# Kernel tuning notes

Measured on AMD Instinct MI355X. Metric: run time of the kernel, lower is better.

Reference implementation:

```python
import jax, jax.numpy as jnp
import numpy as np

N_NODES = 50000


def _gcn_conv(h, src, dst, W, b):
    # h: [N, d_in] -> [N, d_out]; symmetric-normalized aggregation with self-loops
    N = h.shape[0]
    h = h @ W  # transform first (d_out < d_in), like PyG GCNConv
    deg = jax.ops.segment_sum(jnp.ones_like(dst, dtype=h.dtype), dst, num_segments=N)
    dinv = jnp.where(deg > 0, jax.lax.rsqrt(jnp.maximum(deg, 1.0)), 0.0)
    norm = dinv[src] * dinv[dst]  # [E']
    msg = h[src] * norm[:, None]  # [E', d_out]
    out = jax.ops.segment_sum(msg, dst, num_segments=N)
    return out + b


def setup_inputs() -> dict:
    key = jax.random.key(0)
    k1, k2, k3, k4 = jax.random.split(key, 4)
    dim_in, dim_h, dim_out, E = 512, 96, 40, 800000
    x = jax.random.normal(k1, (N_NODES, dim_in), dtype=jnp.float32)
    edge_index = jax.random.randint(k2, (2, E), 0, N_NODES, dtype=jnp.int64)
    W1 = jax.random.normal(k3, (dim_in, dim_h), dtype=jnp.float32) / np.sqrt(dim_in)
    b1 = jnp.zeros((dim_h,), dtype=jnp.float32)
    W2 = jax.random.normal(k4, (dim_h, dim_out), dtype=jnp.float32) / np.sqrt(dim_h)
    b2 = jnp.zeros((dim_out,), dtype=jnp.float32)
    return {"x": x, "edge_index": edge_index, "W1": W1, "b1": b1, "W2": W2, "b2": b2}


def reference(x, edge_index, W1, b1, W2, b2):
    N = x.shape[0]
    loops = jnp.arange(N, dtype=edge_index.dtype)
    src = jnp.concatenate([edge_index[0], loops])
    dst = jnp.concatenate([edge_index[1], loops])
    h = jax.nn.relu(_gcn_conv(x, src, dst, W1, b1))
    # dropout p=0.5 is identity in eval mode (training=False)
    logits = _gcn_conv(h, src, dst, W2, b2)
    return (logits, jax.nn.log_softmax(logits, axis=1))
```

## Files before the change

### kernel.cpp

```cpp
#include <hip/hip_runtime.h>
#include <cstdint>
#include <cstddef>

#define DIN 512
#define DH  96
#define DOUT 40

typedef __attribute__((ext_vector_type(8))) short s8v;
typedef __attribute__((ext_vector_type(4))) float f4v;

__device__ __forceinline__ ushort f2bf(float f) {
    uint u = __float_as_uint(f);
    u += 0x7fffu + ((u >> 16) & 1u);
    return (ushort)(u >> 16);
}
__device__ __forceinline__ float bflo(uint u) { return __uint_as_float(u << 16); }
__device__ __forceinline__ float bfhi(uint u) { return __uint_as_float(u & 0xffff0000u); }

__global__ __launch_bounds__(256) void k_prep(
    const float* __restrict__ W1, const float* __restrict__ W2,
    int* __restrict__ cnt, ushort* __restrict__ W1T, ushort* __restrict__ W2T, int N)
{
    int i = blockIdx.x * 256 + threadIdx.x;
    if (i < N) cnt[i] = 0;
    if (i < DIN * DH) {
        int k = i / DH, n = i % DH;
        W1T[(size_t)n * DIN + k] = f2bf(W1[i]);
    }
    if (i < 48 * DH) {
        int n = i / DH, k = i % DH;
        W2T[i] = (n < DOUT) ? f2bf(W2[(size_t)k * DOUT + n]) : (ushort)0;
    }
}

__global__ __launch_bounds__(256) void k_hist(const int* __restrict__ dst, int* __restrict__ cnt, int E) {
    int e = blockIdx.x * 256 + threadIdx.x;
    if (e < E) atomicAdd(&cnt[dst[e]], 1);
}

__global__ __launch_bounds__(256) void k_blocksum(const int* __restrict__ cnt, int* __restrict__ bsum, int N) {
    int i = blockIdx.x * 256 + threadIdx.x;
    int c = (i < N) ? cnt[i] : 0;
    #pragma unroll
    for (int off = 32; off >= 1; off >>= 1) c += __shfl_down(c, off, 64);
    __shared__ int wsum[4];
    if ((threadIdx.x & 63) == 0) wsum[threadIdx.x >> 6] = c;
    __syncthreads();
    if (threadIdx.x == 0) bsum[blockIdx.x] = wsum[0] + wsum[1] + wsum[2] + wsum[3];
}

__global__ __launch_bounds__(256) void k_scan_small(const int* __restrict__ bsum, int* __restrict__ boff, int SB) {
    __shared__ int p[256];
    int tid = threadIdx.x;
    int v = (tid < SB) ? bsum[tid] : 0;
    p[tid] = v;
    __syncthreads();
    #pragma unroll
    for (int off = 1; off < 256; off <<= 1) {
        int t = (tid >= off) ? p[tid - off] : 0;
        __syncthreads();
        p[tid] += t;
        __syncthreads();
    }
    if (tid < SB) boff[tid] = p[tid] - v;
}

__global__ __launch_bounds__(256) void k_rowptr(
    const int* __restrict__ cnt, const int* __restrict__ boff,
    int* __restrict__ row_ptr, int* __restrict__ cursor,
    float* __restrict__ dinv, int N)
{
    __shared__ int p[256];
    int tid = threadIdx.x;
    int i = blockIdx.x * 256 + tid;
    int c = (i < N) ? cnt[i] : 0;
    p[tid] = c;
    __syncthreads();
    #pragma unroll
    for (int off = 1; off < 256; off <<= 1) {
        int t = (tid >= off) ? p[tid - off] : 0;
        __syncthreads();
        p[tid] += t;
        __syncthreads();
    }
    int excl = p[tid] - c;
    if (i < N) {
        int base = boff[blockIdx.x] + excl;
        row_ptr[i] = base;
        cursor[i]  = base;
        dinv[i] = rsqrtf(1.0f + (float)c);
        if (i == N - 1) row_ptr[N] = base + c;
    }
}

__global__ __launch_bounds__(256) void k_fill(
    const int* __restrict__ src, const int* __restrict__ dst,
    int* __restrict__ cursor, int* __restrict__ adj, int E)
{
    int e = blockIdx.x * 256 + threadIdx.x;
    if (e >= E) return;
    int pos = atomicAdd(&cursor[dst[e]], 1);
    adj[pos] = src[e];
}

#define G1_ASZ 8192
#define G1_BSZ 6144
__global__ __launch_bounds__(256) void k_gemm1(
    const float* __restrict__ x, const ushort* __restrict__ W1T,
    const float* __restrict__ dinv, ushort* __restrict__ hs1, int N)
{
    __shared__ ushort lds[2 * G1_ASZ + 2 * G1_BSZ];
    const int tid = threadIdx.x;
    const int row0 = blockIdx.x * 128;
    const int lane = tid & 63;
    const int w = tid >> 6;
    const int rb = (w >> 1) * 64;
    const int cb = (w & 1) * 48;
    const int lm = lane & 15;
    const int lq = lane >> 4;

    int aof[4][2], bof[3][2];
    #pragma unroll
    for (int i = 0; i < 4; ++i)
        #pragma unroll
        for (int ks = 0; ks < 2; ++ks) {
            int r = rb + i * 16 + lm;
            int c = ks * 32 + lq * 8;
            aof[i][ks] = r * 64 + (c ^ ((r & 7) << 3));
        }
    #pragma unroll
    for (int j = 0; j < 3; ++j)
        #pragma unroll
        for (int ks = 0; ks < 2; ++ks) {
            int n = cb + j * 16 + lm;
            int c = ks * 32 + lq * 8;
            bof[j][ks] = 2 * G1_ASZ + n * 64 + (c ^ ((n & 7) << 3));
        }

    f4v acc[4][3];
    #pragma unroll
    for (int i = 0; i < 4; ++i)
        #pragma unroll
        for (int j = 0; j < 3; ++j) acc[i][j] = (f4v)0.f;

    const int sr = tid >> 1;
    const int scb = (tid & 1) * 32;

    auto stage = [&](int kt, int buf) {
        int k0 = kt * 64;
        int gr = row0 + sr;
        ushort* A = lds + buf * G1_ASZ;
        #pragma unroll
        for (int s = 0; s < 4; ++s) {
            int c = scb + s * 8;
            float4 v0 = make_float4(0.f, 0.f, 0.f, 0.f), v1 = v0;
            if (gr < N) {
                const float* p = &x[(size_t)gr * DIN + k0 + c];
                v0 = *(const float4*)p;
                v1 = *(const float4*)(p + 4);
            }
            uint4 wv;
            wv.x = (uint)f2bf(v0.x) | ((uint)f2bf(v0.y) << 16);
            wv.y = (uint)f2bf(v0.z) | ((uint)f2bf(v0.w) << 16);
            wv.z = (uint)f2bf(v1.x) | ((uint)f2bf(v1.y) << 16);
            wv.w = (uint)f2bf(v1.z) | ((uint)f2bf(v1.w) << 16);
            *(uint4*)&A[sr * 64 + (c ^ ((sr & 7) << 3))] = wv;
        }
        ushort* B = lds + 2 * G1_ASZ + buf * G1_BSZ;
        #pragma unroll
        for (int it = 0; it < 3; ++it) {
            int ss = tid + it * 256;
            int n = ss >> 3, c = (ss & 7) * 8;
            uint4 wv = *(const uint4*)&W1T[(size_t)n * DIN + k0 + c];
            *(uint4*)&B[n * 64 + (c ^ ((n & 7) << 3))] = wv;
        }
    };

    stage(0, 0);
    for (int kt = 0; kt < 8; ++kt) {
        __syncthreads();
        if (kt < 7) stage(kt + 1, (kt + 1) & 1);
        const int ab = (kt & 1) * G1_ASZ;
        const int bb = (kt & 1) * G1_BSZ;
        #pragma unroll
        for (int ks = 0; ks < 2; ++ks) {
            s8v b0 = *(s8v*)&lds[bof[0][ks] + bb];
            s8v b1 = *(s8v*)&lds[bof[1][ks] + bb];
            s8v b2 = *(s8v*)&lds[bof[2][ks] + bb];
            #pragma unroll
            for (int i = 0; i < 4; ++i) {
                s8v a = *(s8v*)&lds[aof[i][ks] + ab];
                acc[i][0] = __builtin_amdgcn_mfma_f32_16x16x32_bf16(a, b0, acc[i][0], 0, 0, 0);
                acc[i][1] = __builtin_amdgcn_mfma_f32_16x16x32_bf16(a, b1, acc[i][1], 0, 0, 0);
                acc[i][2] = __builtin_amdgcn_mfma_f32_16x16x32_bf16(a, b2, acc[i][2], 0, 0, 0);
            }
        }
    }

    #pragma unroll
    for (int i = 0; i < 4; ++i) {
        int gr0 = row0 + rb + i * 16 + lq * 4;
        #pragma unroll
        for (int q = 0; q < 4; ++q) {
            int gr = gr0 + q;
            if (gr < N) {
                float di = dinv[gr];
                #pragma unroll
                for (int j = 0; j < 3; ++j)
                    hs1[(size_t)gr * DH + cb + j * 16 + lm] = f2bf(acc[i][j][q] * di);
            }
        }
    }
}

__global__ __launch_bounds__(256) void k_agg1(
    const int* __restrict__ row_ptr, const int* __restrict__ adj,
    const float* __restrict__ dinv, const ushort* __restrict__ hs1,
    const float* __restrict__ b1, ushort* __restrict__ h1, int N)
{
    int t = blockIdx.x * 256 + threadIdx.x;
    int node = t >> 6, lane = t & 63;
    if (node >= N) return;
    int c = lane << 1;
    const bool act = (c < DH);

    float a0 = 0.f, a1 = 0.f;
    if (act) {
        uint u = *(const uint*)&hs1[(size_t)node * DH + c];
        a0 = bflo(u); a1 = bfhi(u);
    }
    int e = row_ptr[node], e1 = row_ptr[node + 1];
    for (; e + 3 < e1; e += 4) {
        int s0 = adj[e], s1 = adj[e + 1], s2 = adj[e + 2], s3 = adj[e + 3];
        if (act) {
            uint u0 = *(const uint*)&hs1[(size_t)s0 * DH + c];
            uint u1 = *(const uint*)&hs1[(size_t)s1 * DH + c];
            uint u2 = *(const uint*)&hs1[(size_t)s2 * DH + c];
            uint u3 = *(const uint*)&hs1[(size_t)s3 * DH + c];
            a0 += bflo(u0); a1 += bfhi(u0);
            a0 += bflo(u1); a1 += bfhi(u1);
            a0 += bflo(u2); a1 += bfhi(u2);
            a0 += bflo(u3); a1 += bfhi(u3);
        }
    }
    for (; e < e1; ++e) {
        int s = adj[e];
        if (act) {
            uint u = *(const uint*)&hs1[(size_t)s * DH + c];
            a0 += bflo(u); a1 += bfhi(u);
        }
    }
    if (act) {
        float di = dinv[node];
        float r0 = fmaxf(fmaf(a0, di, b1[c]), 0.f);
        float r1 = fmaxf(fmaf(a1, di, b1[c + 1]), 0.f);
        uint wv = (uint)f2bf(r0) | ((uint)f2bf(r1) << 16);
        *(uint*)&h1[(size_t)node * DH + c] = wv;
    }
}

#define G2_HS 16384
__global__ __launch_bounds__(256) void k_gemm2(
    const ushort* __restrict__ h1, const ushort* __restrict__ W2T,
    const float* __restrict__ dinv, float* __restrict__ hs2, int N)
{
    __shared__ ushort lds[G2_HS + 48 * 128];
    const int tid = threadIdx.x;
    const int row0 = blockIdx.x * 128;

    for (int f = tid; f < 576; f += 256) {
        int r = f / 12, c = (f % 12) * 8;
        uint4 v = *(const uint4*)&W2T[r * DH + c];
        *(uint4*)&lds[G2_HS + r * 128 + (c ^ ((r & 7) << 3))] = v;
    }
    {
        int r = tid >> 1, half = tid & 1;
        int gr = row0 + r;
        #pragma unroll
        for (int i = 0; i < 6; ++i) {
            int c = half * 48 + i * 8;
            uint4 v = make_uint4(0, 0, 0, 0);
            if (gr < N) v = *(const uint4*)&h1[(size_t)gr * DH + c];
            *(uint4*)&lds[r * 128 + (c ^ ((r & 7) << 3))] = v;
        }
    }
    __syncthreads();

    const int lane = tid & 63, w = tid >> 6;
    const int rb = w * 32, lm = lane & 15, lq = lane >> 4;
    f4v acc[2][3];
    #pragma unroll
    for (int i = 0; i < 2; ++i)
        #pragma unroll
        for (int j = 0; j < 3; ++j) acc[i][j] = (f4v)0.f;

    #pragma unroll
    for (int ks = 0; ks < 3; ++ks) {
        int kk = ks * 32 + lq * 8;
        s8v b[3];
        #pragma unroll
        for (int j = 0; j < 3; ++j) {
            int n = j * 16 + lm;
            b[j] = *(s8v*)&lds[G2_HS + n * 128 + (kk ^ ((n & 7) << 3))];
        }
        #pragma unroll
        for (int i = 0; i < 2; ++i) {
            int r = rb + i * 16 + lm;
            s8v a = *(s8v*)&lds[r * 128 + (kk ^ ((r & 7) << 3))];
            #pragma unroll
            for (int j = 0; j < 3; ++j)
                acc[i][j] = __builtin_amdgcn_mfma_f32_16x16x32_bf16(a, b[j], acc[i][j], 0, 0, 0);
        }
    }

    #pragma unroll
    for (int i = 0; i < 2; ++i) {
        int gr0 = row0 + rb + i * 16 + lq * 4;
        #pragma unroll
        for (int q = 0; q < 4; ++q) {
            int gr = gr0 + q;
            if (gr < N) {
                float di = dinv[gr];
                #pragma unroll
                for (int j = 0; j < 3; ++j) {
                    int col = j * 16 + lm;
                    if (col < DOUT)
                        hs2[(size_t)gr * DOUT + col] = acc[i][j][q] * di;
                }
            }
        }
    }
}

__global__ __launch_bounds__(256) void k_agg2sm(
    const int* __restrict__ row_ptr, const int* __restrict__ adj,
    const float* __restrict__ dinv, const float* __restrict__ hs2,
    const float* __restrict__ b2, float* __restrict__ out,
    float* __restrict__ lsm, int N)
{
    int t = blockIdx.x * 256 + threadIdx.x;
    int node = t >> 6, lane = t & 63;
    if (node >= N) return;
    const bool act = lane < DOUT;

    float acc = act ? hs2[(size_t)node * DOUT + lane] : 0.f;
    int e = row_ptr[node], e1 = row_ptr[node + 1];
    for (; e + 3 < e1; e += 4) {
        int s0 = adj[e], s1 = adj[e + 1], s2 = adj[e + 2], s3 = adj[e + 3];
        if (act) {
            float v0 = hs2[(size_t)s0 * DOUT + lane];
            float v1 = hs2[(size_t)s1 * DOUT + lane];
            float v2 = hs2[(size_t)s2 * DOUT + lane];
            float v3 = hs2[(size_t)s3 * DOUT + lane];
            acc += v0 + v1 + v2 + v3;
        }
    }
    for (; e < e1; ++e) {
        int s = adj[e];
        if (act) acc += hs2[(size_t)s * DOUT + lane];
    }

    float v = act ? fmaf(acc, dinv[node], b2[lane]) : -1e30f;
    float m = v;
    #pragma unroll
    for (int off = 32; off >= 1; off >>= 1) m = fmaxf(m, __shfl_xor(m, off));
    float ex = act ? __expf(v - m) : 0.f;
    float s = ex;
    #pragma unroll
    for (int off = 32; off >= 1; off >>= 1) s += __shfl_xor(s, off);
    float lse = m + __logf(s);
    if (act) {
        out[(size_t)node * DOUT + lane] = v;
        lsm[(size_t)node * DOUT + lane] = v - lse;
    }
}

extern "C" void kernel_launch(void* const* d_in, const int* in_sizes, int n_in,
                              void* d_out, int out_size, void* d_ws, size_t ws_size,
                              hipStream_t stream) {
    const float* x  = (const float*)d_in[0];
    const int*   ei = (const int*)d_in[1];
    const float* W1 = (const float*)d_in[2];
    const float* b1 = (const float*)d_in[3];
    const float* W2 = (const float*)d_in[4];
    const float* b2 = (const float*)d_in[5];

    const int N = in_sizes[0] / DIN;
    const int E = in_sizes[1] / 2;
    const int* srcp = ei;
    const int* dstp = ei + E;
    const int SB = (N + 255) / 256;

    ushort* hs1 = (ushort*)d_ws;
    ushort* h1  = hs1 + (size_t)N * DH;
    float* hs2  = (float*)(h1 + (size_t)N * DH);
    float* dinv = hs2 + (size_t)N * DOUT;
    ushort* W1T = (ushort*)(dinv + N);
    ushort* W2T = W1T + (size_t)DH * DIN;
    int* cnt     = (int*)(W2T + 48 * DH);
    int* cursor  = cnt + N;
    int* row_ptr = cursor + N;
    int* adj     = row_ptr + N + 1;
    int* bsum    = adj + E;
    int* boff    = bsum + SB;

    float* out = (float*)d_out;
    float* lsm = out + (size_t)N * DOUT;

    const int gE = (E + 255) / 256;

    k_prep<<<SB, 256, 0, stream>>>(W1, W2, cnt, W1T, W2T, N);
    k_hist<<<gE, 256, 0, stream>>>(dstp, cnt, E);
    k_blocksum<<<SB, 256, 0, stream>>>(cnt, bsum, N);
    k_scan_small<<<1, 256, 0, stream>>>(bsum, boff, SB);
    k_rowptr<<<SB, 256, 0, stream>>>(cnt, boff, row_ptr, cursor, dinv, N);
    k_fill<<<gE, 256, 0, stream>>>(srcp, dstp, cursor, adj, E);

    k_gemm1<<<(N + 127) / 128, 256, 0, stream>>>(x, W1T, dinv, hs1, N);
    k_agg1<<<(int)(((size_t)N * 64 + 255) / 256), 256, 0, stream>>>(row_ptr, adj, dinv, hs1, b1, h1, N);

    k_gemm2<<<(N + 127) / 128, 256, 0, stream>>>(h1, W2T, dinv, hs2, N);
    k_agg2sm<<<(int)(((size_t)N * 64 + 255) / 256), 256, 0, stream>>>(row_ptr, adj, dinv, hs2, b2, out, lsm, N);
}
```

Measured before the change: 225.3 us.

## Record histogram slot per edge, unroll gathers by eight, use packed bf16 convert

The histogram kernel now stores each edge's atomic return value as its local slot. The fill kernel then writes adjacency entries without a second atomic pass over cursors, at the cost of an extra E-sized int array. The aggregation gather loops are unrolled from four to eight neighbours to keep more loads in flight. Float-to-bf16 packing switches to the HIP intrinsic for paired conversion.

Result: faster. 185.2 us (-17.8%).

```diff
diff --git a/kernel.cpp b/kernel.cpp
--- a/kernel.cpp
+++ b/kernel.cpp
@@ -1,4 +1,5 @@
 #include <hip/hip_runtime.h>
+#include <hip/hip_bf16.h>
 #include <cstdint>
 #include <cstddef>
 
@@ -13,6 +14,10 @@
     uint u = __float_as_uint(f);
     u += 0x7fffu + ((u >> 16) & 1u);
     return (ushort)(u >> 16);
+}
+__device__ __forceinline__ uint f2bf2(float lo, float hi) {
+    __hip_bfloat162 h = __float22bfloat162_rn(make_float2(lo, hi));
+    return *(uint*)&h;
 }
 __device__ __forceinline__ float bflo(uint u) { return __uint_as_float(u << 16); }
 __device__ __forceinline__ float bfhi(uint u) { return __uint_as_float(u & 0xffff0000u); }
@@ -33,9 +38,11 @@
     }
 }
 
-__global__ __launch_bounds__(256) void k_hist(const int* __restrict__ dst, int* __restrict__ cnt, int E) {
+__global__ __launch_bounds__(256) void k_hist(
+    const int* __restrict__ dst, int* __restrict__ cnt, int* __restrict__ pos, int E)
+{
     int e = blockIdx.x * 256 + threadIdx.x;
-    if (e < E) atomicAdd(&cnt[dst[e]], 1);
+    if (e < E) pos[e] = atomicAdd(&cnt[dst[e]], 1);
 }
 
 __global__ __launch_bounds__(256) void k_blocksum(const int* __restrict__ cnt, int* __restrict__ bsum, int N) {
@@ -67,8 +74,7 @@
 
 __global__ __launch_bounds__(256) void k_rowptr(
     const int* __restrict__ cnt, const int* __restrict__ boff,
-    int* __restrict__ row_ptr, int* __restrict__ cursor,
-    float* __restrict__ dinv, int N)
+    int* __restrict__ row_ptr, float* __restrict__ dinv, int N)
 {
     __shared__ int p[256];
     int tid = threadIdx.x;
@@ -87,7 +93,6 @@
     if (i < N) {
         int base = boff[blockIdx.x] + excl;
         row_ptr[i] = base;
-        cursor[i]  = base;
         dinv[i] = rsqrtf(1.0f + (float)c);
         if (i == N - 1) row_ptr[N] = base + c;
     }
@@ -95,46 +100,39 @@
 
 __global__ __launch_bounds__(256) void k_fill(
     const int* __restrict__ src, const int* __restrict__ dst,
-    int* __restrict__ cursor, int* __restrict__ adj, int E)
+    const int* __restrict__ row_ptr, const int* __restrict__ pos,
+    int* __restrict__ adj, int E)
 {
     int e = blockIdx.x * 256 + threadIdx.x;
     if (e >= E) return;
-    int pos = atomicAdd(&cursor[dst[e]], 1);
-    adj[pos] = src[e];
-}
-
-#define G1_ASZ 8192
-#define G1_BSZ 6144
+    adj[row_ptr[dst[e]] + pos[e]] = src[e];
+}
+
 __global__ __launch_bounds__(256) void k_gemm1(
     const float* __restrict__ x, const ushort* __restrict__ W1T,
     const float* __restrict__ dinv, ushort* __restrict__ hs1, int N)
 {
-    __shared__ ushort lds[2 * G1_ASZ + 2 * G1_BSZ];
+    __shared__ __align__(16) ushort lds[28672];
     const int tid = threadIdx.x;
     const int row0 = blockIdx.x * 128;
-    const int lane = tid & 63;
-    const int w = tid >> 6;
-    const int rb = (w >> 1) * 64;
-    const int cb = (w & 1) * 48;
-    const int lm = lane & 15;
-    const int lq = lane >> 4;
+    const int lane = tid & 63, w = tid >> 6;
+    const int rb = (w >> 1) * 64, cb = (w & 1) * 48;
+    const int lm = lane & 15, lq = lane >> 4;
 
     int aof[4][2], bof[3][2];
     #pragma unroll
     for (int i = 0; i < 4; ++i)
         #pragma unroll
         for (int ks = 0; ks < 2; ++ks) {
-            int r = rb + i * 16 + lm;
-            int c = ks * 32 + lq * 8;
+            int r = rb + i * 16 + lm, c = ks * 32 + lq * 8;
             aof[i][ks] = r * 64 + (c ^ ((r & 7) << 3));
         }
     #pragma unroll
     for (int j = 0; j < 3; ++j)
         #pragma unroll
         for (int ks = 0; ks < 2; ++ks) {
-            int n = cb + j * 16 + lm;
-            int c = ks * 32 + lq * 8;
-            bof[j][ks] = 2 * G1_ASZ + n * 64 + (c ^ ((n & 7) << 3));
+            int n = cb + j * 16 + lm, c = ks * 32 + lq * 8;
+            bof[j][ks] = 16384 + n * 64 + (c ^ ((n & 7) << 3));
         }
 
     f4v acc[4][3];
@@ -143,30 +141,29 @@
         #pragma unroll
         for (int j = 0; j < 3; ++j) acc[i][j] = (f4v)0.f;
 
-    const int sr = tid >> 1;
-    const int scb = (tid & 1) * 32;
+    const int sr = tid >> 1, scb = (tid & 1) * 32;
 
     auto stage = [&](int kt, int buf) {
         int k0 = kt * 64;
         int gr = row0 + sr;
-        ushort* A = lds + buf * G1_ASZ;
+        ushort* A = lds + buf * 8192;
         #pragma unroll
         for (int s = 0; s < 4; ++s) {
             int c = scb + s * 8;
             float4 v0 = make_float4(0.f, 0.f, 0.f, 0.f), v1 = v0;
             if (gr < N) {
-                const float* p = &x[(size_t)gr * DIN + k0 + c];
-                v0 = *(const float4*)p;
-                v1 = *(const float4*)(p + 4);
+                const float* pp = &x[(size_t)gr * DIN + k0 + c];
+                v0 = *(const float4*)pp;
+                v1 = *(const float4*)(pp + 4);
             }
             uint4 wv;
-            wv.x = (uint)f2bf(v0.x) | ((uint)f2bf(v0.y) << 16);
-            wv.y = (uint)f2bf(v0.z) | ((uint)f2bf(v0.w) << 16);
-            wv.z = (uint)f2bf(v1.x) | ((uint)f2bf(v1.y) << 16);
-            wv.w = (uint)f2bf(v1.z) | ((uint)f2bf(v1.w) << 16);
+            wv.x = f2bf2(v0.x, v0.y);
+            wv.y = f2bf2(v0.z, v0.w);
+            wv.z = f2bf2(v1.x, v1.y);
+            wv.w = f2bf2(v1.z, v1.w);
             *(uint4*)&A[sr * 64 + (c ^ ((sr & 7) << 3))] = wv;
         }
-        ushort* B = lds + 2 * G1_ASZ + buf * G1_BSZ;
+        ushort* B = lds + 16384 + buf * 6144;
         #pragma unroll
         for (int it = 0; it < 3; ++it) {
             int ss = tid + it * 256;
@@ -180,8 +177,8 @@
     for (int kt = 0; kt < 8; ++kt) {
         __syncthreads();
         if (kt < 7) stage(kt + 1, (kt + 1) & 1);
-        const int ab = (kt & 1) * G1_ASZ;
-        const int bb = (kt & 1) * G1_BSZ;
+        const int ab = (kt & 1) * 8192;
+        const int bb = (kt & 1) * 6144;
         #pragma unroll
         for (int ks = 0; ks < 2; ++ks) {
             s8v b0 = *(s8v*)&lds[bof[0][ks] + bb];
@@ -230,17 +227,26 @@
         a0 = bflo(u); a1 = bfhi(u);
     }
     int e = row_ptr[node], e1 = row_ptr[node + 1];
-    for (; e + 3 < e1; e += 4) {
-        int s0 = adj[e], s1 = adj[e + 1], s2 = adj[e + 2], s3 = adj[e + 3];
+    for (; e + 7 < e1; e += 8) {
+        int s0 = adj[e],     s1 = adj[e + 1], s2 = adj[e + 2], s3 = adj[e + 3];
+        int s4 = adj[e + 4], s5 = adj[e + 5], s6 = adj[e + 6], s7 = adj[e + 7];
         if (act) {
             uint u0 = *(const uint*)&hs1[(size_t)s0 * DH + c];
             uint u1 = *(const uint*)&hs1[(size_t)s1 * DH + c];
             uint u2 = *(const uint*)&hs1[(size_t)s2 * DH + c];
             uint u3 = *(const uint*)&hs1[(size_t)s3 * DH + c];
+            uint u4 = *(const uint*)&hs1[(size_t)s4 * DH + c];
+            uint u5 = *(const uint*)&hs1[(size_t)s5 * DH + c];
+            uint u6 = *(const uint*)&hs1[(size_t)s6 * DH + c];
+            uint u7 = *(const uint*)&hs1[(size_t)s7 * DH + c];
             a0 += bflo(u0); a1 += bfhi(u0);
             a0 += bflo(u1); a1 += bfhi(u1);
             a0 += bflo(u2); a1 += bfhi(u2);
             a0 += bflo(u3); a1 += bfhi(u3);
+            a0 += bflo(u4); a1 += bfhi(u4);
+            a0 += bflo(u5); a1 += bfhi(u5);
+            a0 += bflo(u6); a1 += bfhi(u6);
+            a0 += bflo(u7); a1 += bfhi(u7);
         }
     }
     for (; e < e1; ++e) {
@@ -254,24 +260,22 @@
         float di = dinv[node];
         float r0 = fmaxf(fmaf(a0, di, b1[c]), 0.f);
         float r1 = fmaxf(fmaf(a1, di, b1[c + 1]), 0.f);
-        uint wv = (uint)f2bf(r0) | ((uint)f2bf(r1) << 16);
-        *(uint*)&h1[(size_t)node * DH + c] = wv;
-    }
-}
-
-#define G2_HS 16384
+        *(uint*)&h1[(size_t)node * DH + c] = f2bf2(r0, r1);
+    }
+}
+
 __global__ __launch_bounds__(256) void k_gemm2(
     const ushort* __restrict__ h1, const ushort* __restrict__ W2T,
     const float* __restrict__ dinv, float* __restrict__ hs2, int N)
 {
-    __shared__ ushort lds[G2_HS + 48 * 128];
+    __shared__ __align__(16) ushort lds[16384 + 48 * 128];
     const int tid = threadIdx.x;
     const int row0 = blockIdx.x * 128;
 
     for (int f = tid; f < 576; f += 256) {
         int r = f / 12, c = (f % 12) * 8;
         uint4 v = *(const uint4*)&W2T[r * DH + c];
-        *(uint4*)&lds[G2_HS + r * 128 + (c ^ ((r & 7) << 3))] = v;
+        *(uint4*)&lds[16384 + r * 128 + (c ^ ((r & 7) << 3))] = v;
     }
     {
         int r = tid >> 1, half = tid & 1;
@@ -301,7 +305,7 @@
         #pragma unroll
         for (int j = 0; j < 3; ++j) {
             int n = j * 16 + lm;
-            b[j] = *(s8v*)&lds[G2_HS + n * 128 + (kk ^ ((n & 7) << 3))];
+            b[j] = *(s8v*)&lds[16384 + n * 128 + (kk ^ ((n & 7) << 3))];
         }
         #pragma unroll
         for (int i = 0; i < 2; ++i) {
@@ -345,14 +349,19 @@
 
     float acc = act ? hs2[(size_t)node * DOUT + lane] : 0.f;
     int e = row_ptr[node], e1 = row_ptr[node + 1];
-    for (; e + 3 < e1; e += 4) {
-        int s0 = adj[e], s1 = adj[e + 1], s2 = adj[e + 2], s3 = adj[e + 3];
+    for (; e + 7 < e1; e += 8) {
+        int s0 = adj[e],     s1 = adj[e + 1], s2 = adj[e + 2], s3 = adj[e + 3];
+        int s4 = adj[e + 4], s5 = adj[e + 5], s6 = adj[e + 6], s7 = adj[e + 7];
         if (act) {
             float v0 = hs2[(size_t)s0 * DOUT + lane];
             float v1 = hs2[(size_t)s1 * DOUT + lane];
             float v2 = hs2[(size_t)s2 * DOUT + lane];
             float v3 = hs2[(size_t)s3 * DOUT + lane];
-            acc += v0 + v1 + v2 + v3;
+            float v4 = hs2[(size_t)s4 * DOUT + lane];
+            float v5 = hs2[(size_t)s5 * DOUT + lane];
+            float v6 = hs2[(size_t)s6 * DOUT + lane];
+            float v7 = hs2[(size_t)s7 * DOUT + lane];
+            acc += ((v0 + v1) + (v2 + v3)) + ((v4 + v5) + (v6 + v7));
         }
     }
     for (; e < e1; ++e) {
@@ -398,10 +407,10 @@
     ushort* W1T = (ushort*)(dinv + N);
     ushort* W2T = W1T + (size_t)DH * DIN;
     int* cnt     = (int*)(W2T + 48 * DH);
-    int* cursor  = cnt + N;
-    int* row_ptr = cursor + N;
+    int* row_ptr = cnt + N;
     int* adj     = row_ptr + N + 1;
-    int* bsum    = adj + E;
+    int* pos     = adj + E;
+    int* bsum    = pos + E;
     int* boff    = bsum + SB;
 
     float* out = (float*)d_out;
@@ -410,11 +419,11 @@
     const int gE = (E + 255) / 256;
 
     k_prep<<<SB, 256, 0, stream>>>(W1, W2, cnt, W1T, W2T, N);
-    k_hist<<<gE, 256, 0, stream>>>(dstp, cnt, E);
+    k_hist<<<gE, 256, 0, stream>>>(dstp, cnt, pos, E);
     k_blocksum<<<SB, 256, 0, stream>>>(cnt, bsum, N);
     k_scan_small<<<1, 256, 0, stream>>>(bsum, boff, SB);
-    k_rowptr<<<SB, 256, 0, stream>>>(cnt, boff, row_ptr, cursor, dinv, N);
-    k_fill<<<gE, 256, 0, stream>>>(srcp, dstp, cursor, adj, E);
+    k_rowptr<<<SB, 256, 0, stream>>>(cnt, boff, row_ptr, dinv, N);
+    k_fill<<<gE, 256, 0, stream>>>(srcp, dstp, row_ptr, pos, adj, E);
 
     k_gemm1<<<(N + 127) / 128, 256, 0, stream>>>(x, W1T, dinv, hs1, N);
     k_agg1<<<(int)(((size_t)N * 64 + 255) / 256), 256, 0, stream>>>(row_ptr, adj, dinv, hs1, b1, h1, N);
```
